# Optimization experiments

Hardware: AMD Instinct MI355X
Metric: run time of the kernel (lower is better)

Reference implementation:

```python
import jax, jax.numpy as jnp
import numpy as np
from jax import lax

# Model dims (from init_kwargs / mamba_ssm defaults)
D_MODEL = 256
EXPAND = 2
D_INNER = EXPAND * D_MODEL      # 512
D_STATE = 64                     # ssm_rank
DT_RANK = D_MODEL // 16          # 16 (mamba_ssm default ceil(d_model/16))
D_CONV = 4
IMG = 384
PATCH = 16
BATCH = 16
NUM_CLASSES = 10
NBLK = 6                         # sum(depths) = 2+2+2
GRID = IMG // PATCH
NTOK = GRID * GRID + 1           # 577 (patches + cls token)


def setup_inputs() -> dict:
    key = jax.random.key(0)
    ks = iter(jax.random.split(key, 32))
    rn = lambda shape, s=0.02: jax.random.normal(next(ks), shape, jnp.float32) * s
    inp = {}
    inp["x"] = jax.random.normal(next(ks), (BATCH, 3, IMG, IMG), jnp.float32)
    # patch embed conv
    inp["patch_w"] = rn((D_MODEL, 3, PATCH, PATCH), 0.05)
    inp["patch_b"] = jnp.zeros((D_MODEL,), jnp.float32)
    inp["cls_token"] = rn((1, 1, D_MODEL))
    inp["pos_embed"] = rn((1, NTOK, D_MODEL))
    # stacked per-block Mamba params
    inp["norm_w"] = jnp.ones((NBLK, D_MODEL), jnp.float32)
    inp["norm_b"] = jnp.zeros((NBLK, D_MODEL), jnp.float32)
    inp["in_proj_w"] = rn((NBLK, 2 * D_INNER, D_MODEL))
    inp["conv_w"] = rn((NBLK, D_INNER, 1, D_CONV), 0.1)
    inp["conv_b"] = jnp.zeros((NBLK, D_INNER), jnp.float32)
    inp["x_proj_w"] = rn((NBLK, DT_RANK + 2 * D_STATE, D_INNER))
    inp["dt_proj_w"] = rn((NBLK, D_INNER, DT_RANK), 0.1)
    inp["dt_proj_b"] = rn((NBLK, D_INNER), 0.5)
    # S4D-real init: A = -[1..d_state]
    inp["A_log"] = jnp.log(jnp.broadcast_to(
        jnp.arange(1, D_STATE + 1, dtype=jnp.float32), (NBLK, D_INNER, D_STATE)))
    inp["D_ssm"] = jnp.ones((NBLK, D_INNER), jnp.float32)
    inp["out_proj_w"] = rn((NBLK, D_MODEL, D_INNER))
    inp["fnorm_w"] = jnp.ones((D_MODEL,), jnp.float32)
    inp["fnorm_b"] = jnp.zeros((D_MODEL,), jnp.float32)
    inp["head_w"] = rn((NUM_CLASSES, D_MODEL))
    inp["head_b"] = jnp.zeros((NUM_CLASSES,), jnp.float32)
    return inp


def layer_norm(x, w, b, eps=1e-5):
    mu = jnp.mean(x, axis=-1, keepdims=True)
    var = jnp.mean(jnp.square(x - mu), axis=-1, keepdims=True)
    return (x - mu) * lax.rsqrt(var + eps) * w + b


def causal_dwconv(x, w, b):
    # x: (B, di, L), w: (di, 1, K) depthwise; causal left pad K-1
    K = w.shape[-1]
    y = lax.conv_general_dilated(x, w, (1,), [(K - 1, 0)],
                                 dimension_numbers=("NCH", "OIH", "NCH"),
                                 feature_group_count=x.shape[1])
    return y + b[None, :, None]


def selective_scan(u, dt, A, Bm, Cm, Dp):
    # u, dt: (B, L, di); Bm, Cm: (B, L, ds); A: (di, ds); Dp: (di,)
    def step(h, inp):
        dt_t, B_t, C_t, u_t = inp                       # (B,di),(B,ds),(B,ds),(B,di)
        dA = jnp.exp(dt_t[:, :, None] * A)              # (B, di, ds)
        h = dA * h + (dt_t * u_t)[:, :, None] * B_t[:, None, :]
        y = jnp.einsum('bds,bs->bd', h, C_t)
        return h, y
    h0 = jnp.zeros((u.shape[0], A.shape[0], A.shape[1]), u.dtype)
    _, ys = lax.scan(step, h0, (dt.transpose(1, 0, 2), Bm.transpose(1, 0, 2),
                                Cm.transpose(1, 0, 2), u.transpose(1, 0, 2)))
    return ys.transpose(1, 0, 2) + u * Dp


def mamba_block(x, nw, nb, inw, cw, cb, xpw, dtw, dtb, alog, dp, ow):
    res = x
    x = layer_norm(x, nw, nb)
    xz = jnp.einsum('bld,ed->ble', x, inw)              # (B, L, 2*di)
    xi, z = jnp.split(xz, 2, axis=-1)
    xi = causal_dwconv(xi.transpose(0, 2, 1), cw, cb).transpose(0, 2, 1)
    xi = jax.nn.silu(xi)
    dbl = jnp.einsum('bld,ed->ble', xi, xpw)            # (B, L, dt_rank + 2*ds)
    dtr = dbl[..., :DT_RANK]
    Bm = dbl[..., DT_RANK:DT_RANK + D_STATE]
    Cm = dbl[..., DT_RANK + D_STATE:]
    dt = jax.nn.softplus(jnp.einsum('blr,dr->bld', dtr, dtw) + dtb)
    A = -jnp.exp(alog)
    y = selective_scan(xi, dt, A, Bm, Cm, dp)
    y = y * jax.nn.silu(z)
    return res + jnp.einsum('bld,ed->ble', y, ow)


def reference(x, patch_w, patch_b, cls_token, pos_embed,
              norm_w, norm_b, in_proj_w, conv_w, conv_b, x_proj_w,
              dt_proj_w, dt_proj_b, A_log, D_ssm, out_proj_w,
              fnorm_w, fnorm_b, head_w, head_b):
    B = x.shape[0]
    h = lax.conv_general_dilated(x, patch_w, (PATCH, PATCH), 'VALID',
                                 dimension_numbers=("NCHW", "OIHW", "NCHW"))
    h = h + patch_b[None, :, None, None]
    h = h.reshape(B, D_MODEL, -1).transpose(0, 2, 1)    # (B, G*G, D)
    h = jnp.concatenate([jnp.broadcast_to(cls_token, (B, 1, D_MODEL)), h], axis=1)
    h = h + pos_embed
    for i in range(NBLK):
        h = mamba_block(h, norm_w[i], norm_b[i], in_proj_w[i], conv_w[i], conv_b[i],
                        x_proj_w[i], dt_proj_w[i], dt_proj_b[i], A_log[i], D_ssm[i],
                        out_proj_w[i])
    h = layer_norm(h, fnorm_w, fnorm_b)
    return h[:, 0] @ head_w.T + head_b
```

## Files before the change

### kernel.cpp

```cpp
#include <hip/hip_runtime.h>
#include <hip/hip_bf16.h>
#include <cstdint>
#include <cstddef>

#define L_TOK 577
#define DM 256
#define DI 512
#define DS_ 64
#define NROWS (16*577)
#define PROWS (16*576)

typedef float f32x4v __attribute__((ext_vector_type(4)));
typedef __bf16 bf16x8 __attribute__((ext_vector_type(8)));

__device__ __forceinline__ float fast_exp2(float x) {
#if __has_builtin(__builtin_amdgcn_exp2f)
    return __builtin_amdgcn_exp2f(x);
#else
    return __expf(x * 0.6931471805599453f);
#endif
}

__global__ __launch_bounds__(256)
void k_gemm(const float* __restrict__ A, int lda,
            const float* __restrict__ B, int ldb,
            float* __restrict__ C, int ldc,
            int M, int N, int K, int beta)
{
    __shared__ char sA[128*64*2];
    __shared__ char sB[128*64*2];
    const int tid  = threadIdx.x;
    const int lane = tid & 63;
    const int wave = tid >> 6;
    const int wr = wave >> 1, wc = wave & 1;
    const int tm = blockIdx.y * 128, tn = blockIdx.x * 128;

    f32x4v acc[4][4];
#pragma unroll
    for (int m = 0; m < 4; ++m)
#pragma unroll
        for (int n = 0; n < 4; ++n) acc[m][n] = (f32x4v){0.f, 0.f, 0.f, 0.f};

    const int nk = K >> 6;
    for (int kt = 0; kt < nk; ++kt) {
        const int k0 = kt << 6;
        __syncthreads();
#pragma unroll
        for (int i = 0; i < 4; ++i) {
            int c = tid + (i << 8);
            int row = c >> 3, slot = c & 7;
            int gr = tm + row; gr = gr < M ? gr : M - 1;
            const float* src = A + (size_t)gr * lda + k0 + (slot << 3);
            float4 lo = *reinterpret_cast<const float4*>(src);
            float4 hi = *reinterpret_cast<const float4*>(src + 4);
            bf16x8 pk;
            pk[0]=(__bf16)lo.x; pk[1]=(__bf16)lo.y; pk[2]=(__bf16)lo.z; pk[3]=(__bf16)lo.w;
            pk[4]=(__bf16)hi.x; pk[5]=(__bf16)hi.y; pk[6]=(__bf16)hi.z; pk[7]=(__bf16)hi.w;
            *reinterpret_cast<bf16x8*>(&sA[(row << 7) + ((slot ^ (row & 7)) << 4)]) = pk;
        }
#pragma unroll
        for (int i = 0; i < 4; ++i) {
            int c = tid + (i << 8);
            int row = c >> 3, slot = c & 7;
            int gr = tn + row; gr = gr < N ? gr : N - 1;
            const float* src = B + (size_t)gr * ldb + k0 + (slot << 3);
            float4 lo = *reinterpret_cast<const float4*>(src);
            float4 hi = *reinterpret_cast<const float4*>(src + 4);
            bf16x8 pk;
            pk[0]=(__bf16)lo.x; pk[1]=(__bf16)lo.y; pk[2]=(__bf16)lo.z; pk[3]=(__bf16)lo.w;
            pk[4]=(__bf16)hi.x; pk[5]=(__bf16)hi.y; pk[6]=(__bf16)hi.z; pk[7]=(__bf16)hi.w;
            *reinterpret_cast<bf16x8*>(&sB[(row << 7) + ((slot ^ (row & 7)) << 4)]) = pk;
        }
        __syncthreads();

        bf16x8 af[4][2], bfr[4][2];
#pragma unroll
        for (int kk = 0; kk < 2; ++kk) {
            int sl = (kk << 2) + (lane >> 4);
#pragma unroll
            for (int m = 0; m < 4; ++m) {
                int row = (wr << 6) + (m << 4) + (lane & 15);
                af[m][kk] = *reinterpret_cast<const bf16x8*>(&sA[(row << 7) + ((sl ^ (row & 7)) << 4)]);
            }
#pragma unroll
            for (int n = 0; n < 4; ++n) {
                int row = (wc << 6) + (n << 4) + (lane & 15);
                bfr[n][kk] = *reinterpret_cast<const bf16x8*>(&sB[(row << 7) + ((sl ^ (row & 7)) << 4)]);
            }
        }
#pragma unroll
        for (int kk = 0; kk < 2; ++kk)
#pragma unroll
            for (int m = 0; m < 4; ++m)
#pragma unroll
                for (int n = 0; n < 4; ++n)
                    acc[m][n] = __builtin_amdgcn_mfma_f32_16x16x32_bf16(af[m][kk], bfr[n][kk], acc[m][n], 0, 0, 0);
    }

#pragma unroll
    for (int m = 0; m < 4; ++m) {
        int grow0 = tm + (wr << 6) + (m << 4) + ((lane >> 4) << 2);
#pragma unroll
        for (int n = 0; n < 4; ++n) {
            int gcol = tn + (wc << 6) + (n << 4) + (lane & 15);
            if (gcol < N) {
#pragma unroll
                for (int j = 0; j < 4; ++j) {
                    int grow = grow0 + j;
                    if (grow < M) {
                        size_t o = (size_t)grow * ldc + gcol;
                        float v = acc[m][n][j];
                        if (beta) v += C[o];
                        C[o] = v;
                    }
                }
            }
        }
    }
}

__global__ __launch_bounds__(256)
void k_im2col(const float* __restrict__ x, float* __restrict__ xcol)
{
    int id = blockIdx.x * 256 + threadIdx.x;
    int kh = id & 15;
    int ci = (id >> 4) % 3;
    int row = id / 48;
    int b = row / 576, p = row % 576;
    int py = p / 24, px = p % 24;
    const float* src = x + ((size_t)(b*3 + ci)*384 + py*16 + kh)*384 + px*16;
    float* dst = xcol + (size_t)row*768 + ci*256 + kh*16;
#pragma unroll
    for (int j = 0; j < 4; ++j)
        *reinterpret_cast<float4*>(dst + j*4) = *reinterpret_cast<const float4*>(src + j*4);
}

__global__ __launch_bounds__(256)
void k_assemble(const float* __restrict__ Ctmp, const float* __restrict__ pb,
                const float* __restrict__ cls, const float* __restrict__ pos,
                float* __restrict__ h_tok)
{
    int i4 = blockIdx.x * 256 + threadIdx.x;
    int c4 = i4 & 63;
    int tok = (i4 >> 6) % 577;
    int b = i4 / (577*64);
    float4 pv = *reinterpret_cast<const float4*>(pos + tok*256 + c4*4);
    float4 r;
    if (tok == 0) {
        float4 cv = *reinterpret_cast<const float4*>(cls + c4*4);
        r.x = cv.x + pv.x; r.y = cv.y + pv.y; r.z = cv.z + pv.z; r.w = cv.w + pv.w;
    } else {
        float4 t = *reinterpret_cast<const float4*>(Ctmp + (size_t)(b*576 + tok - 1)*256 + c4*4);
        float4 bb = *reinterpret_cast<const float4*>(pb + c4*4);
        r.x = t.x + bb.x + pv.x; r.y = t.y + bb.y + pv.y;
        r.z = t.z + bb.z + pv.z; r.w = t.w + bb.w + pv.w;
    }
    *reinterpret_cast<float4*>(h_tok + (size_t)i4*4) = r;
}

__global__ __launch_bounds__(256)
void k_ln(const float* __restrict__ X, const float* __restrict__ w,
          const float* __restrict__ bb, float* __restrict__ O)
{
    int lane = threadIdx.x & 63;
    int row = blockIdx.x * 4 + (threadIdx.x >> 6);
    const float4 v = *reinterpret_cast<const float4*>(X + (size_t)row*256 + lane*4);
    float s1 = v.x + v.y + v.z + v.w;
    float s2 = v.x*v.x + v.y*v.y + v.z*v.z + v.w*v.w;
#pragma unroll
    for (int o2 = 32; o2; o2 >>= 1) { s1 += __shfl_xor(s1, o2); s2 += __shfl_xor(s2, o2); }
    float mu = s1 * (1.f/256.f);
    float var = s2 * (1.f/256.f) - mu*mu;
    float rs = rsqrtf(var + 1e-5f);
    float4 wv = *reinterpret_cast<const float4*>(w + lane*4);
    float4 bv = *reinterpret_cast<const float4*>(bb + lane*4);
    float4 o;
    o.x = (v.x - mu)*rs*wv.x + bv.x;
    o.y = (v.y - mu)*rs*wv.y + bv.y;
    o.z = (v.z - mu)*rs*wv.z + bv.z;
    o.w = (v.w - mu)*rs*wv.w + bv.w;
    *reinterpret_cast<float4*>(O + (size_t)row*256 + lane*4) = o;
}

__global__ __launch_bounds__(256)
void k_conv(const float* __restrict__ xz, const float* __restrict__ cw,
            const float* __restrict__ cb, float* __restrict__ xi)
{
    int gw = blockIdx.x * 4 + (threadIdx.x >> 6);
    int lane = threadIdx.x & 63;
    int tc = gw % 73;
    int eg = (gw / 73) & 7;
    int b  = gw / (73*8);
    int e = eg*64 + lane;
    float4 wv = *reinterpret_cast<const float4*>(cw + e*4);
    float bias = cb[e];
    int t0 = tc * 8;
    float xv[11];
#pragma unroll
    for (int j = 0; j < 11; ++j) {
        int t = t0 - 3 + j;
        xv[j] = (t >= 0 && t < 577) ? xz[(size_t)(b*577 + t)*1024 + e] : 0.f;
    }
#pragma unroll
    for (int j = 0; j < 8; ++j) {
        int t = t0 + j;
        if (t < 577) {
            float a = wv.x*xv[j] + wv.y*xv[j+1] + wv.z*xv[j+2] + wv.w*xv[j+3] + bias;
            float sgm = 1.f / (1.f + __expf(-a));
            xi[(size_t)(b*577 + t)*512 + e] = a * sgm;
        }
    }
}

__global__ __launch_bounds__(256)
void k_dtfuse(const float* __restrict__ dbl, const float* __restrict__ dtw,
              const float* __restrict__ dtb, const float* __restrict__ xi,
              float* __restrict__ tri2)
{
    int row = blockIdx.x >> 1;
    int e = ((blockIdx.x & 1) << 8) + threadIdx.x;
    const float* dr = dbl + (size_t)row*144;
    const float* wp = dtw + e*16;
    float accv = dtb[e];
#pragma unroll
    for (int r = 0; r < 16; r += 4) {
        float4 wv = *reinterpret_cast<const float4*>(wp + r);
        accv += wv.x*dr[r] + wv.y*dr[r+1] + wv.z*dr[r+2] + wv.w*dr[r+3];
    }
    float sp = accv > 20.f ? accv : log1pf(__expf(accv));
    float u = xi[(size_t)row*512 + e];
    float2 o; o.x = sp; o.y = sp * u;
    *reinterpret_cast<float2*>(tri2 + ((size_t)row*512 + e)*2) = o;
}

__global__ __launch_bounds__(256, 6)
void k_scan(const float* __restrict__ tri2, const float* __restrict__ dbl,
            const float* __restrict__ A_log, float* __restrict__ y)
{
    __shared__ float bc[16*128];
    __shared__ float tp[4*16*65];
    const int tid  = threadIdx.x;
    const int lane = tid & 63;
    const int wv   = tid >> 6;
    const int bb   = blockIdx.x >> 7;
    const int d    = __builtin_amdgcn_readfirstlane(((blockIdx.x & 127) << 2) + wv);
    const float alog2 = -__expf(A_log[(size_t)d*64 + lane]) * 1.44269504f;
    const size_t row0 = (size_t)bb * 577;
    const float2* trip = reinterpret_cast<const float2*>(tri2) + row0*512 + d;
    const float* dblb = dbl + row0*144 + 16;
    float* yp = y + row0*512 + d;
    float* tpw = tp + wv*(16*65);
    const int j0 = tid >> 5, q = tid & 31;
    float h = 0.f;

    for (int c = 0; c < 36; ++c) {
        const int t0 = c << 4;
        __syncthreads();
        {
            const float* s0 = dblb + (size_t)(t0 + j0)*144 + q*4;
            const float* s1 = dblb + (size_t)(t0 + j0 + 8)*144 + q*4;
            float4 v0 = *reinterpret_cast<const float4*>(s0);
            float4 v1 = *reinterpret_cast<const float4*>(s1);
            *reinterpret_cast<float4*>(&bc[j0*128 + q*4]) = v0;
            *reinterpret_cast<float4*>(&bc[(j0+8)*128 + q*4]) = v1;
        }
        __syncthreads();
        float p[16];
#pragma unroll
        for (int j = 0; j < 16; ++j) {
            float2 tr = trip[(size_t)(t0 + j)*512];
            float Bv = bc[j*128 + lane];
            float Cv = bc[j*128 + 64 + lane];
            float dA = fast_exp2(tr.x * alog2);
            h = __builtin_fmaf(dA, h, tr.y * Bv);
            p[j] = h * Cv;
        }
#pragma unroll
        for (int j = 0; j < 16; ++j) tpw[j*65 + lane] = p[j];
        float partial = 0.f;
        {
            const int g = lane >> 4, tt = lane & 15;
            const float* rp = tpw + tt*65 + g*16;
#pragma unroll
            for (int k = 0; k < 16; ++k) partial += rp[k];
        }
        partial += __shfl_xor(partial, 16);
        partial += __shfl_xor(partial, 32);
        if (lane < 16) yp[(size_t)(t0 + lane)*512] = partial;
    }
    {
        float2 tr = trip[(size_t)576*512];
        float Bv = dblb[(size_t)576*144 + lane];
        float Cv = dblb[(size_t)576*144 + 64 + lane];
        float dA = fast_exp2(tr.x * alog2);
        h = __builtin_fmaf(dA, h, tr.y * Bv);
        float p = h * Cv;
        p += __shfl_xor(p, 32); p += __shfl_xor(p, 16); p += __shfl_xor(p, 8);
        p += __shfl_xor(p, 4);  p += __shfl_xor(p, 2);  p += __shfl_xor(p, 1);
        if (lane == 0) yp[(size_t)576*512] = p;
    }
}

__global__ __launch_bounds__(256)
void k_gate(float* __restrict__ y, const float* __restrict__ xz,
            const float* __restrict__ xi, const float* __restrict__ Dp)
{
    int i4 = blockIdx.x * 256 + threadIdx.x;
    int row = i4 >> 7;
    int c4 = i4 & 127;
    float4 yv = *reinterpret_cast<float4*>(y + (size_t)i4*4);
    float4 uv = *reinterpret_cast<const float4*>(xi + (size_t)i4*4);
    float4 dv = *reinterpret_cast<const float4*>(Dp + c4*4);
    const float4 zv = *reinterpret_cast<const float4*>(xz + (size_t)row*1024 + 512 + c4*4);
    float4 o;
    o.x = (yv.x + uv.x*dv.x) * (zv.x / (1.f + __expf(-zv.x)));
    o.y = (yv.y + uv.y*dv.y) * (zv.y / (1.f + __expf(-zv.y)));
    o.z = (yv.z + uv.z*dv.z) * (zv.z / (1.f + __expf(-zv.z)));
    o.w = (yv.w + uv.w*dv.w) * (zv.w / (1.f + __expf(-zv.w)));
    *reinterpret_cast<float4*>(y + (size_t)i4*4) = o;
}

__global__ __launch_bounds__(256)
void k_head(const float* __restrict__ h_tok, const float* __restrict__ fw,
            const float* __restrict__ fb, const float* __restrict__ hw,
            const float* __restrict__ hb, float* __restrict__ out)
{
    int b = blockIdx.x, tid = threadIdx.x;
    __shared__ float sv[256];
    __shared__ float sr[16];
    float v = h_tok[(size_t)b*577*256 + tid];
    float s1 = v, s2 = v*v;
#pragma unroll
    for (int o2 = 32; o2; o2 >>= 1) { s1 += __shfl_xor(s1, o2); s2 += __shfl_xor(s2, o2); }
    int wave = tid >> 6;
    if ((tid & 63) == 0) { sr[wave] = s1; sr[wave + 8] = s2; }
    __syncthreads();
    float t1 = sr[0] + sr[1] + sr[2] + sr[3];
    float t2 = sr[8] + sr[9] + sr[10] + sr[11];
    float mu = t1 * (1.f/256.f);
    float var = t2 * (1.f/256.f) - mu*mu;
    float rs = rsqrtf(var + 1e-5f);
    sv[tid] = (v - mu)*rs*fw[tid] + fb[tid];
    __syncthreads();
    if (tid < 10) {
        float acc = hb[tid];
        for (int d2 = 0; d2 < 256; ++d2) acc += sv[d2]*hw[tid*256 + d2];
        out[b*10 + tid] = acc;
    }
}

extern "C" void kernel_launch(void* const* d_in, const int* in_sizes, int n_in,
                              void* d_out, int out_size, void* d_ws, size_t ws_size,
                              hipStream_t stream)
{
    const float* x         = (const float*)d_in[0];
    const float* patch_w   = (const float*)d_in[1];
    const float* patch_b   = (const float*)d_in[2];
    const float* cls_tok   = (const float*)d_in[3];
    const float* pos_emb   = (const float*)d_in[4];
    const float* norm_w    = (const float*)d_in[5];
    const float* norm_b    = (const float*)d_in[6];
    const float* in_proj_w = (const float*)d_in[7];
    const float* conv_w    = (const float*)d_in[8];
    const float* conv_b    = (const float*)d_in[9];
    const float* x_proj_w  = (const float*)d_in[10];
    const float* dt_proj_w = (const float*)d_in[11];
    const float* dt_proj_b = (const float*)d_in[12];
    const float* A_log     = (const float*)d_in[13];
    const float* D_ssm     = (const float*)d_in[14];
    const float* out_proj_w= (const float*)d_in[15];
    const float* fnorm_w   = (const float*)d_in[16];
    const float* fnorm_b   = (const float*)d_in[17];
    const float* head_w    = (const float*)d_in[18];
    const float* head_b    = (const float*)d_in[19];
    float* out = (float*)d_out;

    char* ws = (char*)d_ws;
    size_t off = 0;
    auto carve = [&](size_t bytes) -> float* {
        float* p = (float*)(ws + off);
        off += (bytes + 255) & ~(size_t)255;
        return p;
    };
    float* h_tok = carve((size_t)NROWS*DM*4);
    float* xln   = carve((size_t)NROWS*DM*4);
    float* xz    = carve((size_t)NROWS*1024*4);
    float* xi    = carve((size_t)NROWS*DI*4);
    float* dbl   = carve((size_t)NROWS*144*4);
    float* tri2  = carve((size_t)NROWS*DI*2*4);
    float* yb    = carve((size_t)NROWS*DI*4);
    float* xcol  = xz;
    float* Ctmp  = xi;

    k_im2col<<<1728, 256, 0, stream>>>(x, xcol);
    {
        dim3 g(2, 72);
        k_gemm<<<g, 256, 0, stream>>>(xcol, 768, patch_w, 768, Ctmp, 256, PROWS, 256, 768, 0);
    }
    k_assemble<<<2308, 256, 0, stream>>>(Ctmp, patch_b, cls_tok, pos_emb, h_tok);

    for (int i = 0; i < 6; ++i) {
        k_ln<<<2308, 256, 0, stream>>>(h_tok, norm_w + i*DM, norm_b + i*DM, xln);
        {
            dim3 g(8, 73);
            k_gemm<<<g, 256, 0, stream>>>(xln, DM, in_proj_w + (size_t)i*1024*DM, DM,
                                          xz, 1024, NROWS, 1024, DM, 0);
        }
        k_conv<<<2336, 256, 0, stream>>>(xz, conv_w + (size_t)i*DI*4, conv_b + i*DI, xi);
        {
            dim3 g(2, 73);
            k_gemm<<<g, 256, 0, stream>>>(xi, DI, x_proj_w + (size_t)i*144*DI, DI,
                                          dbl, 144, NROWS, 144, DI, 0);
        }
        k_dtfuse<<<NROWS*2, 256, 0, stream>>>(dbl, dt_proj_w + (size_t)i*DI*16, dt_proj_b + i*DI,
                                              xi, tri2);
        k_scan<<<2048, 256, 0, stream>>>(tri2, dbl, A_log + (size_t)i*DI*DS_, yb);
        k_gate<<<4616, 256, 0, stream>>>(yb, xz, xi, D_ssm + i*DI);
        {
            dim3 g(2, 73);
            k_gemm<<<g, 256, 0, stream>>>(yb, DI, out_proj_w + (size_t)i*DM*DI, DI,
                                          h_tok, DM, NROWS, DM, DI, 1);
        }
    }
    k_head<<<16, 256, 0, stream>>>(h_tok, fnorm_w, fnorm_b, head_w, head_b, out);
}
```

Baseline: 1.886 ms.

## Chunk-major tri2 layout so scan reads contiguous per-channel chunks

The dt/softplus kernel now handles 16 timesteps per block: it stages the dt-rank inputs in shared memory and writes tri2 in a chunked layout (batch, chunk, channel, 16 steps), so each scan wave reads one contiguous 128-byte run per chunk instead of strided float2s. The scan kernel drops its shared-memory B/C staging and both per-chunk __syncthreads, and reads B and C straight from global memory. This cuts the block count of the dt kernel and the barrier overhead in the scan. In exchange, the B/C loads are now issued by every wave rather than shared through LDS, and the dt kernel's output stores become strided per thread.

```diff
diff --git a/kernel.cpp b/kernel.cpp
--- a/kernel.cpp
+++ b/kernel.cpp
@@ -9,6 +9,7 @@
 #define DS_ 64
 #define NROWS (16*577)
 #define PROWS (16*576)
+#define NCH 37
 
 typedef float f32x4v __attribute__((ext_vector_type(4)));
 typedef __bf16 bf16x8 __attribute__((ext_vector_type(8)));
@@ -217,27 +218,44 @@
               const float* __restrict__ dtb, const float* __restrict__ xi,
               float* __restrict__ tri2)
 {
-    int row = blockIdx.x >> 1;
-    int e = ((blockIdx.x & 1) << 8) + threadIdx.x;
-    const float* dr = dbl + (size_t)row*144;
+    __shared__ float dtr[16][16];
+    const int tid = threadIdx.x;
+    const int b    = blockIdx.x / 74;
+    const int rr   = blockIdx.x % 74;
+    const int tc   = rr >> 1;
+    const int e    = ((rr & 1) << 8) + tid;
+    const int nj   = (tc == 36) ? 1 : 16;
+    {
+        int j = tid >> 4, r = tid & 15;
+        if (tid < 256 && j < nj)
+            dtr[j][r] = dbl[((size_t)(b*577) + tc*16 + j)*144 + r];
+    }
+    __syncthreads();
     const float* wp = dtw + e*16;
-    float accv = dtb[e];
-#pragma unroll
-    for (int r = 0; r < 16; r += 4) {
-        float4 wv = *reinterpret_cast<const float4*>(wp + r);
-        accv += wv.x*dr[r] + wv.y*dr[r+1] + wv.z*dr[r+2] + wv.w*dr[r+3];
-    }
-    float sp = accv > 20.f ? accv : log1pf(__expf(accv));
-    float u = xi[(size_t)row*512 + e];
-    float2 o; o.x = sp; o.y = sp * u;
-    *reinterpret_cast<float2*>(tri2 + ((size_t)row*512 + e)*2) = o;
+    float4 w0 = *reinterpret_cast<const float4*>(wp);
+    float4 w1 = *reinterpret_cast<const float4*>(wp + 4);
+    float4 w2 = *reinterpret_cast<const float4*>(wp + 8);
+    float4 w3 = *reinterpret_cast<const float4*>(wp + 12);
+    float bias = dtb[e];
+    float* outp = tri2 + ((size_t)(b*37 + tc)*512 + e)*32;
+    for (int j = 0; j < nj; ++j) {
+        const float* dr = dtr[j];
+        float accv = bias;
+        accv += w0.x*dr[0] + w0.y*dr[1] + w0.z*dr[2] + w0.w*dr[3];
+        accv += w1.x*dr[4] + w1.y*dr[5] + w1.z*dr[6] + w1.w*dr[7];
+        accv += w2.x*dr[8] + w2.y*dr[9] + w2.z*dr[10] + w2.w*dr[11];
+        accv += w3.x*dr[12] + w3.y*dr[13] + w3.z*dr[14] + w3.w*dr[15];
+        float sp = accv > 20.f ? accv : log1pf(__expf(accv));
+        float u = xi[((size_t)(b*577) + tc*16 + j)*512 + e];
+        float2 o; o.x = sp; o.y = sp * u;
+        *reinterpret_cast<float2*>(outp + j*2) = o;
+    }
 }
 
 __global__ __launch_bounds__(256, 6)
 void k_scan(const float* __restrict__ tri2, const float* __restrict__ dbl,
             const float* __restrict__ A_log, float* __restrict__ y)
 {
-    __shared__ float bc[16*128];
     __shared__ float tp[4*16*65];
     const int tid  = threadIdx.x;
     const int lane = tid & 63;
@@ -245,32 +263,22 @@
     const int bb   = blockIdx.x >> 7;
     const int d    = __builtin_amdgcn_readfirstlane(((blockIdx.x & 127) << 2) + wv);
     const float alog2 = -__expf(A_log[(size_t)d*64 + lane]) * 1.44269504f;
-    const size_t row0 = (size_t)bb * 577;
-    const float2* trip = reinterpret_cast<const float2*>(tri2) + row0*512 + d;
-    const float* dblb = dbl + row0*144 + 16;
-    float* yp = y + row0*512 + d;
+    const float2* trp = reinterpret_cast<const float2*>(tri2)
+                      + ((size_t)bb*NCH*512 + d)*16;
+    const float* Bb = dbl + (size_t)bb*577*144 + 16 + lane;
+    float* yp = y + (size_t)bb*577*512 + d;
     float* tpw = tp + wv*(16*65);
-    const int j0 = tid >> 5, q = tid & 31;
+    const int g = lane >> 4, tt = lane & 15;
     float h = 0.f;
 
     for (int c = 0; c < 36; ++c) {
         const int t0 = c << 4;
-        __syncthreads();
-        {
-            const float* s0 = dblb + (size_t)(t0 + j0)*144 + q*4;
-            const float* s1 = dblb + (size_t)(t0 + j0 + 8)*144 + q*4;
-            float4 v0 = *reinterpret_cast<const float4*>(s0);
-            float4 v1 = *reinterpret_cast<const float4*>(s1);
-            *reinterpret_cast<float4*>(&bc[j0*128 + q*4]) = v0;
-            *reinterpret_cast<float4*>(&bc[(j0+8)*128 + q*4]) = v1;
-        }
-        __syncthreads();
         float p[16];
 #pragma unroll
         for (int j = 0; j < 16; ++j) {
-            float2 tr = trip[(size_t)(t0 + j)*512];
-            float Bv = bc[j*128 + lane];
-            float Cv = bc[j*128 + 64 + lane];
+            float2 tr = trp[(size_t)c*8192 + j];
+            float Bv = Bb[(size_t)(t0 + j)*144];
+            float Cv = Bb[(size_t)(t0 + j)*144 + 64];
             float dA = fast_exp2(tr.x * alog2);
             h = __builtin_fmaf(dA, h, tr.y * Bv);
             p[j] = h * Cv;
@@ -279,19 +287,18 @@
         for (int j = 0; j < 16; ++j) tpw[j*65 + lane] = p[j];
         float partial = 0.f;
         {
-            const int g = lane >> 4, tt = lane & 15;
             const float* rp = tpw + tt*65 + g*16;
 #pragma unroll
             for (int k = 0; k < 16; ++k) partial += rp[k];
         }
         partial += __shfl_xor(partial, 16);
         partial += __shfl_xor(partial, 32);
-        if (lane < 16) yp[(size_t)(t0 + lane)*512] = partial;
+        if (lane < 16) yp[(size_t)(t0 + tt)*512] = partial;
     }
     {
-        float2 tr = trip[(size_t)576*512];
-        float Bv = dblb[(size_t)576*144 + lane];
-        float Cv = dblb[(size_t)576*144 + 64 + lane];
+        float2 tr = trp[(size_t)36*8192];
+        float Bv = Bb[(size_t)576*144];
+        float Cv = Bb[(size_t)576*144 + 64];
         float dA = fast_exp2(tr.x * alog2);
         h = __builtin_fmaf(dA, h, tr.y * Bv);
         float p = h * Cv;
@@ -387,7 +394,7 @@
     float* xz    = carve((size_t)NROWS*1024*4);
     float* xi    = carve((size_t)NROWS*DI*4);
     float* dbl   = carve((size_t)NROWS*144*4);
-    float* tri2  = carve((size_t)NROWS*DI*2*4);
+    float* tri2  = carve((size_t)16*NCH*DI*32*4);
     float* yb    = carve((size_t)NROWS*DI*4);
     float* xcol  = xz;
     float* Ctmp  = xi;
@@ -412,8 +419,8 @@
             k_gemm<<<g, 256, 0, stream>>>(xi, DI, x_proj_w + (size_t)i*144*DI, DI,
                                           dbl, 144, NROWS, 144, DI, 0);
         }
-        k_dtfuse<<<NROWS*2, 256, 0, stream>>>(dbl, dt_proj_w + (size_t)i*DI*16, dt_proj_b + i*DI,
-                                              xi, tri2);
+        k_dtfuse<<<16*NCH*2, 256, 0, stream>>>(dbl, dt_proj_w + (size_t)i*DI*16, dt_proj_b + i*DI,
+                                               xi, tri2);
         k_scan<<<2048, 256, 0, stream>>>(tri2, dbl, A_log + (size_t)i*DI*DS_, yb);
         k_gate<<<4616, 256, 0, stream>>>(yb, xz, xi, D_ssm + i*DI);
         {
```

Result: faster. 1.846 ms (-2.2%).
